# Kernel tuning notes

Hardware: AMD Instinct MI355X
Metric: run time of the kernel (lower is better)

Reference implementation:

```python
import jax, jax.numpy as jnp
import numpy as np

Q, B, D, NH, DH, DI, M = 1024, 4, 1024, 16, 64, 4096, 1024
K = Q + M  # klen
SCALE_W = 0.02
LN_EPS = 1e-5


def _layer_norm(x, g, b):
    mu = jnp.mean(x, axis=-1, keepdims=True)
    var = jnp.var(x, axis=-1, keepdims=True)
    return (x - mu) * jax.lax.rsqrt(var + LN_EPS) * g + b


def _rel_shift(x):
    # x: [qlen, klen, bsz, n_head] -> Transformer-XL relative shift
    q, k = x.shape[0], x.shape[1]
    zero_pad = jnp.zeros((q, 1) + x.shape[2:], x.dtype)
    x_padded = jnp.concatenate([zero_pad, x], axis=1)          # [q, k+1, b, n]
    x_padded = x_padded.reshape((k + 1, q) + x.shape[2:])      # [k+1, q, b, n]
    return x_padded[1:].reshape(x.shape)


def setup_inputs() -> dict:
    key = jax.random.key(0)
    ks = jax.random.split(key, 12)
    f32 = jnp.float32
    inp = {
        "w": jax.random.normal(ks[0], (Q, B, D), f32),
        "r": jax.random.normal(ks[1], (K, 1, D), f32),
        "mems": jax.random.normal(ks[2], (M, B, D), f32),
        "qkv_w": SCALE_W * jax.random.normal(ks[3], (D, 3 * NH * DH), f32),
        "r_net_w": SCALE_W * jax.random.normal(ks[4], (D, NH * DH), f32),
        "o_w": SCALE_W * jax.random.normal(ks[5], (NH * DH, D), f32),
        "r_w_bias": SCALE_W * jax.random.normal(ks[6], (NH, DH), f32),
        "r_r_bias": SCALE_W * jax.random.normal(ks[7], (NH, DH), f32),
        "ln1_g": jnp.ones((D,), f32),
        "ln1_b": jnp.zeros((D,), f32),
        "ff_w1": SCALE_W * jax.random.normal(ks[8], (D, DI), f32),
        "ff_b1": jnp.zeros((DI,), f32),
        "ff_w2": SCALE_W * jax.random.normal(ks[9], (DI, D), f32),
        "ff_b2": jnp.zeros((D,), f32),
        "ln2_g": jnp.ones((D,), f32),
        "ln2_b": jnp.zeros((D,), f32),
        # causal mask with memory: query i attends to keys j <= i + mem_len
        "attn_mask": jnp.arange(K)[None, :] > (jnp.arange(Q)[:, None] + M),
    }
    return inp


def reference(w, r, mems, qkv_w, r_net_w, o_w, r_w_bias, r_r_bias,
              ln1_g, ln1_b, ff_w1, ff_b1, ff_w2, ff_b2, ln2_g, ln2_b,
              attn_mask):
    qlen, bsz = w.shape[0], w.shape[1]
    # --- relative multi-head attention (post-lnorm, mems concat) ---
    cat = jnp.concatenate([mems, w], axis=0)                   # [klen, b, d]
    w_heads = cat @ qkv_w                                      # [klen, b, 3*nh*dh]
    r_head_k = (r @ r_net_w).reshape(-1, NH, DH)               # [rlen, nh, dh]
    q_h, k_h, v_h = jnp.split(w_heads, 3, axis=-1)
    klen = k_h.shape[0]
    q_h = q_h[-qlen:].reshape(qlen, bsz, NH, DH)
    k_h = k_h.reshape(klen, bsz, NH, DH)
    v_h = v_h.reshape(klen, bsz, NH, DH)

    rw_q = q_h + r_w_bias[None, None]                          # [q, b, nh, dh]
    AC = jnp.einsum('ibnd,jbnd->ijbn', rw_q, k_h)
    rr_q = q_h + r_r_bias[None, None]
    BD = jnp.einsum('ibnd,jnd->ijbn', rr_q, r_head_k)
    BD = _rel_shift(BD)

    scale = 1.0 / (DH ** 0.5)
    attn_score = (AC + BD) * scale                             # [q, k, b, nh]
    attn_score = jnp.where(attn_mask[:, :, None, None], -jnp.inf, attn_score)
    attn_prob = jax.nn.softmax(attn_score, axis=1)
    attn_vec = jnp.einsum('ijbn,jbnd->ibnd', attn_prob, v_h)
    attn_out = attn_vec.reshape(qlen, bsz, NH * DH) @ o_w      # [q, b, d]
    out = _layer_norm(w + attn_out, ln1_g, ln1_b)

    # --- position-wise FFN (post-lnorm) ---
    core = jax.nn.relu(out @ ff_w1 + ff_b1) @ ff_w2 + ff_b2
    out = _layer_norm(out + core, ln2_g, ln2_b)
    return out
```

## Files before the change

### kernel.cpp

```cpp
#include <hip/hip_runtime.h>
#include <math.h>


#define QLEN 1024
#define BSZ  4
#define DMODEL 1024
#define NHEAD 16
#define DHEAD 64
#define DINNER 4096
#define MEMLEN 1024
#define KLEN 2048

typedef __attribute__((ext_vector_type(8))) short short8;
typedef __attribute__((ext_vector_type(4))) short short4_t;
typedef __attribute__((ext_vector_type(4))) float f32x4;

__device__ __forceinline__ unsigned short f2bf(float x) {
  union { float f; unsigned u; } cv; cv.f = x;
  const unsigned u = cv.u;
  return (unsigned short)((u + 0x7FFFu + ((u >> 16) & 1u)) >> 16);
}
__device__ __forceinline__ float bf2f(unsigned short b) {
  union { unsigned u; float f; } cv; cv.u = ((unsigned)b) << 16;
  return cv.f;
}

__device__ __forceinline__ void gload16(const void* g, void* l) {
  __builtin_amdgcn_global_load_lds(
      (const __attribute__((address_space(1))) unsigned int*)g,
      (__attribute__((address_space(3))) unsigned int*)l, 16, 0, 0);
}

__device__ __forceinline__ int chidx(int row, int kc) {
  return row * 4 + (kc ^ ((row >> 1) & 3));
}

template<int MODE, int TN>
__global__ __launch_bounds__(256) void mgemm(
    const unsigned short* __restrict__ A, const unsigned short* __restrict__ Bt,
    float* __restrict__ C, unsigned short* __restrict__ Cb,
    const float* __restrict__ aux, const float* __restrict__ res,
    unsigned short* __restrict__ oK, unsigned short* __restrict__ oV,
    int Kdim, int N)
{
  constexpr int BUF = 8192 + TN * 64;
  __shared__ __align__(16) char smem[2 * BUF];

  const int tid = threadIdx.x;
  const int lane = tid & 63, wv = tid >> 6;

  const int gx = (int)gridDim.x;
  const int nwg = gx * (int)gridDim.y;
  const int flat = (int)blockIdx.y * gx + (int)blockIdx.x;
  const int swz = (flat & 7) * (nwg >> 3) + (flat >> 3);
  const int m0 = (swz / gx) * 128, n0 = (swz % gx) * TN;

  const unsigned short *gA0, *gA1, *gB0, *gB1 = nullptr;
  {
    int c = tid, m = c >> 2, kc = (c & 3) ^ ((m >> 1) & 3);
    gA0 = A + (size_t)(m0 + m) * Kdim + kc * 8;
    c = 256 + tid; m = c >> 2; kc = (c & 3) ^ ((m >> 1) & 3);
    gA1 = A + (size_t)(m0 + m) * Kdim + kc * 8;
    c = tid; int nn = c >> 2; kc = (c & 3) ^ ((nn >> 1) & 3);
    gB0 = Bt + (size_t)(n0 + nn) * Kdim + kc * 8;
    if constexpr (TN == 128) {
      c = 256 + tid; nn = c >> 2; kc = (c & 3) ^ ((nn >> 1) & 3);
      gB1 = Bt + (size_t)(n0 + nn) * Kdim + kc * 8;
    }
  }
  const int wvoff = (tid & 192) * 16;

  const int fr = lane & 15, kq = lane >> 4;
  constexpr int NJ = TN / 32;
  int aoff[4], boff[NJ];
#pragma unroll
  for (int t = 0; t < 4; ++t) {
    const int ra = (wv & 1) * 64 + t * 16 + fr;
    aoff[t] = chidx(ra, kq) * 16;
  }
#pragma unroll
  for (int t = 0; t < NJ; ++t) {
    const int rb = (wv >> 1) * (TN / 2) + t * 16 + fr;
    boff[t] = 8192 + chidx(rb, kq) * 16;
  }

  f32x4 acc[4][NJ] = {};

  {
    char* const b0 = smem + wvoff;
    gload16(gA0, b0);
    gload16(gA1, b0 + 4096);
    gload16(gB0, b0 + 8192);
    if constexpr (TN == 128) gload16(gB1, b0 + 12288);
    gA0 += 32; gA1 += 32; gB0 += 32;
    if constexpr (TN == 128) gB1 += 32;
  }

  int cur = 0;
  for (int k0 = 0; k0 < Kdim; k0 += 32) {
    if (k0 + 32 < Kdim) {
      char* const nb = smem + (cur ^ 1) * BUF + wvoff;
      gload16(gA0, nb);
      gload16(gA1, nb + 4096);
      gload16(gB0, nb + 8192);
      if constexpr (TN == 128) gload16(gB1, nb + 12288);
      gA0 += 32; gA1 += 32; gB0 += 32;
      if constexpr (TN == 128) gB1 += 32;
      if constexpr (TN == 128)
        asm volatile("s_waitcnt vmcnt(4)" ::: "memory");
      else
        asm volatile("s_waitcnt vmcnt(3)" ::: "memory");
    } else {
      asm volatile("s_waitcnt vmcnt(0)" ::: "memory");
    }
    __builtin_amdgcn_s_barrier();

    const char* const cb = smem + cur * BUF;
    short8 af[4], bfr[NJ];
#pragma unroll
    for (int t = 0; t < 4; ++t) af[t] = *(const short8*)(cb + aoff[t]);
#pragma unroll
    for (int t = 0; t < NJ; ++t) bfr[t] = *(const short8*)(cb + boff[t]);
#pragma unroll
    for (int i = 0; i < 4; ++i)
#pragma unroll
      for (int j = 0; j < NJ; ++j)
        acc[i][j] = __builtin_amdgcn_mfma_f32_16x16x32_bf16(
            af[i], bfr[j], acc[i][j], 0, 0, 0);

    asm volatile("s_waitcnt lgkmcnt(0)" ::: "memory");
    __builtin_amdgcn_s_barrier();
    cur ^= 1;
  }

  const int rbase = m0 + (wv & 1) * 64 + (lane >> 4) * 4;
  const int cbase = n0 + (wv >> 1) * (TN / 2) + (lane & 15);
#pragma unroll
  for (int i = 0; i < 4; ++i) {
#pragma unroll
    for (int r = 0; r < 4; ++r) {
      const int grow = rbase + i * 16 + r;
#pragma unroll
      for (int j = 0; j < NJ; ++j) {
        const int gcol = cbase + j * 16;
        const float v = acc[i][j][r];
        if constexpr (MODE == 0) {
          const int kkg = grow >> 2, b2 = grow & 3;
          const int sec = gcol >> 10, hn = (gcol >> 6) & 15, d = gcol & 63;
          const unsigned short bv = f2bf(v);
          if (sec == 0) {
            if (kkg >= MEMLEN)
              Cb[((size_t)(b2 * NHEAD + hn) * QLEN + (kkg - MEMLEN)) * DHEAD + d] = bv;
          } else if (sec == 1) {
            oK[((size_t)(b2 * NHEAD + hn) * KLEN + kkg) * DHEAD + d] = bv;
          } else {
            oV[((size_t)(b2 * NHEAD + hn) * KLEN + kkg) * DHEAD + d] = bv;
          }
        } else if constexpr (MODE == 1) {
          const int hn = gcol >> 6, d = gcol & 63;
          Cb[((size_t)hn * KLEN + grow) * DHEAD + d] = f2bf(v);
        } else if constexpr (MODE == 2) {
          C[(size_t)grow * N + gcol] = v + res[(size_t)grow * N + gcol];
        } else if constexpr (MODE == 3) {
          Cb[(size_t)grow * N + gcol] = f2bf(fmaxf(v + aux[gcol], 0.f));
        } else {
          C[(size_t)grow * N + gcol] = v + aux[gcol] + res[(size_t)grow * N + gcol];
        }
      }
    }
  }
}

__global__ __launch_bounds__(256) void transpose_v(
    const unsigned short* __restrict__ Vh, unsigned short* __restrict__ Vt)
{
  __shared__ unsigned short t[64 * 80];
  const int j0 = (int)blockIdx.x * 64;
  const int bn = (int)blockIdx.y;
  const int tid = threadIdx.x;
#pragma unroll
  for (int it = 0; it < 2; ++it) {
    const int f = it * 256 + tid;
    const int j = f >> 3, d8 = (f & 7) * 8;
    const short8 v = *(const short8*)(Vh + ((size_t)bn * KLEN + j0 + j) * DHEAD + d8);
    *(short8*)(t + j * 80 + d8) = v;
  }
  __syncthreads();
  const int d = tid >> 2, jseg = (tid & 3) * 16;
  short8 o0, o1;
#pragma unroll
  for (int e = 0; e < 8; ++e) o0[e] = (short)t[(jseg + e) * 80 + d];
#pragma unroll
  for (int e = 0; e < 8; ++e) o1[e] = (short)t[(jseg + 8 + e) * 80 + d];
  unsigned short* op = Vt + ((size_t)bn * DHEAD + d) * KLEN + j0 + jseg;
  *(short8*)op = o0;
  *(short8*)(op + 8) = o1;
}

__global__ __launch_bounds__(256) void cast_all(
    const float* __restrict__ mems, const float* __restrict__ w,
    const float* __restrict__ r, unsigned short* __restrict__ Xcat,
    unsigned short* __restrict__ Rb16)
{
  const size_t i = ((size_t)blockIdx.x * 256 + threadIdx.x) * 8;
  const float* src;
  unsigned short* dst;
  if (i < 4194304)       { src = mems + i;          dst = Xcat + i; }
  else if (i < 8388608)  { src = w + (i - 4194304); dst = Xcat + i; }
  else                   { src = r + (i - 8388608); dst = Rb16 + (i - 8388608); }
  const float4 x = *(const float4*)src;
  const float4 y = *(const float4*)(src + 4);
  short8 v;
  v[0] = (short)f2bf(x.x); v[1] = (short)f2bf(x.y);
  v[2] = (short)f2bf(x.z); v[3] = (short)f2bf(x.w);
  v[4] = (short)f2bf(y.x); v[5] = (short)f2bf(y.y);
  v[6] = (short)f2bf(y.z); v[7] = (short)f2bf(y.w);
  *(short8*)dst = v;
}

__global__ __launch_bounds__(256) void transpose_all(
    const float* __restrict__ qkv_w, const float* __restrict__ r_net_w,
    const float* __restrict__ o_w, const float* __restrict__ ff_w1,
    const float* __restrict__ ff_w2,
    unsigned short* __restrict__ Wqkv, unsigned short* __restrict__ Wr,
    unsigned short* __restrict__ Wo, unsigned short* __restrict__ W1,
    unsigned short* __restrict__ W2)
{
  const int bid = (int)blockIdx.x;
  const float* in; unsigned short* out; int R, C, xt, loc;
  if (bid < 768)        { in = qkv_w;   out = Wqkv; R = 1024; C = 3072; xt = 48; loc = bid; }
  else if (bid < 1024)  { in = r_net_w; out = Wr;   R = 1024; C = 1024; xt = 16; loc = bid - 768; }
  else if (bid < 1280)  { in = o_w;     out = Wo;   R = 1024; C = 1024; xt = 16; loc = bid - 1024; }
  else if (bid < 2304)  { in = ff_w1;   out = W1;   R = 1024; C = 4096; xt = 64; loc = bid - 1280; }
  else                  { in = ff_w2;   out = W2;   R = 4096; C = 1024; xt = 16; loc = bid - 2304; }
  const int c0 = (loc % xt) * 64, r0 = (loc / xt) * 64;

  __shared__ float t[64][65];
  const int tid = threadIdx.x;
  const int rr = tid >> 4, cc = (tid & 15) * 4;
#pragma unroll
  for (int it = 0; it < 4; ++it) {
    const int rw = rr + it * 16;
    const float4 v = *(const float4*)(in + (size_t)(r0 + rw) * C + c0 + cc);
    t[rw][cc] = v.x; t[rw][cc + 1] = v.y; t[rw][cc + 2] = v.z; t[rw][cc + 3] = v.w;
  }
  __syncthreads();
  const int oc = tid >> 2, ob = (tid & 3) * 16;
#pragma unroll
  for (int j4 = 0; j4 < 4; ++j4) {
    short4_t o;
#pragma unroll
    for (int j = 0; j < 4; ++j) o[j] = (short)f2bf(t[ob + j4 * 4 + j][oc]);
    *(short4_t*)(out + (size_t)(c0 + oc) * R + r0 + ob + j4 * 4) = o;
  }
}

__global__ __launch_bounds__(256, 2) void attn_mfma(
    const unsigned short* __restrict__ Qh, const unsigned short* __restrict__ Kh,
    const unsigned short* __restrict__ Vt, const unsigned short* __restrict__ Rk,
    const float* __restrict__ rwb, const float* __restrict__ rrb,
    float* __restrict__ Opart0, float* __restrict__ Opart1,
    float* __restrict__ den0, float* __restrict__ den1)
{
  __shared__ __align__(16) char smem[65536];

  const int tid = threadIdx.x;
  const int lane = tid & 63, wv = tid >> 6;
  const int quad = lane >> 4, l15 = lane & 15;

  const int bid0 = (int)blockIdx.y * 32 + (int)blockIdx.x;
  const int slot = bid0 >> 3;
  const int bn = (bid0 & 7) * 8 + (slot >> 5);
  const int inner = slot & 31;
  const int it = inner >> 1, sp = inner & 1;
  const int i0 = it * 64;
  const int n = bn & 15;

  const int nch = 17 + it;
  const int h = (nch + 1) >> 1;
  const int lo = sp ? h : 0, hi = sp ? nch : h;

  const unsigned short* __restrict__ Qb = Qh + (size_t)bn * QLEN * DHEAD;
  const unsigned short* __restrict__ Kb = Kh + (size_t)bn * KLEN * DHEAD;
  const unsigned short* __restrict__ Vb = Vt + (size_t)bn * DHEAD * KLEN;
  const unsigned short* __restrict__ Rb = Rk + (size_t)n * KLEN * DHEAD;

  short8 qk[2], qr[2];
  {
    const int qrow = i0 + wv * 16 + l15;
    const unsigned short* qp = Qb + (size_t)qrow * DHEAD + quad * 8;
    const float* wp = rwb + n * DHEAD + quad * 8;
    const float* rp = rrb + n * DHEAD + quad * 8;
#pragma unroll
    for (int ks = 0; ks < 2; ++ks) {
      const short8 q8 = *(const short8*)(qp + ks * 32);
#pragma unroll
      for (int e = 0; e < 8; ++e) {
        const float qv = bf2f((unsigned short)q8[e]);
        qk[ks][e] = (short)f2bf(qv + wp[ks * 32 + e]);
        qr[ks][e] = (short)f2bf(qv + rp[ks * 32 + e]);
      }
    }
  }

  int srcl[4];
  bool condE[4];
#pragma unroll
  for (int r = 0; r < 4; ++r) {
    const int E = l15 - quad * 4 - r + 15;
    srcl[r] = (lane & 48) | (E & 15);
    condE[r] = (E >= 16);
  }

  f32x4 O[4] = {};
  float rden[4] = {0.f, 0.f, 0.f, 0.f};
  const int wvoff = (tid & 192) * 16;

  {
    const int j0 = lo * 64;
    const int g64 = lo - it + 15;
    const int rb3 = (g64 % 3) * 64;
#pragma unroll
    for (int t2 = 0; t2 < 2; ++t2) {
      const int s = t2 * 256 + tid;
      const int row = s >> 3, kc = (s & 7) ^ (row & 7);
      gload16(Kb + (((size_t)(j0 + row)) << 6) + kc * 8,
              smem + t2 * 4096 + wvoff);
    }
#pragma unroll
    for (int t2 = 0; t2 < 2; ++t2) {
      const int s = t2 * 256 + tid;
      const int row = s >> 3, kc = (s & 7) ^ (row & 7);
      gload16(Vb + (((size_t)row) << 11) + j0 + kc * 8,
              smem + 16384 + t2 * 4096 + wvoff);
    }
    const int gw = j0 - i0 + 960;
#pragma unroll
    for (int t2 = 0; t2 < 4; ++t2) {
      const int rr = t2 * 32 + (tid >> 3);
      const int gr = gw + rr;
      const int kc = (tid & 7) ^ (rr & 7);
      int pb = rb3 + t2 * 32; if (pb >= 192) pb -= 192;
      gload16(Rb + (((size_t)gr) << 6) + kc * 8,
              smem + 32768 + pb * 128 + wvoff);
    }
  }

  int cur = 0;
  for (int ch = lo; ch < hi; ++ch) {
    const int j0 = ch * 64;
    const int g64 = ch - it + 15;
    const int rb3 = (g64 % 3) * 64;
    const int gw = j0 - i0 + 960;

    asm volatile("s_waitcnt lgkmcnt(0)" ::: "memory");
    __builtin_amdgcn_s_barrier();

    if (ch + 1 < hi) {
      const int nb = cur ^ 1;
      const int j0n = j0 + 64;
#pragma unroll
      for (int t2 = 0; t2 < 2; ++t2) {
        const int s = t2 * 256 + tid;
        const int row = s >> 3, kc = (s & 7) ^ (row & 7);
        gload16(Kb + (((size_t)(j0n + row)) << 6) + kc * 8,
                smem + nb * 8192 + t2 * 4096 + wvoff);
      }
#pragma unroll
      for (int t2 = 0; t2 < 2; ++t2) {
        const int s = t2 * 256 + tid;
        const int row = s >> 3, kc = (s & 7) ^ (row & 7);
        gload16(Vb + (((size_t)row) << 11) + j0n + kc * 8,
                smem + 16384 + nb * 8192 + t2 * 4096 + wvoff);
      }
#pragma unroll
      for (int t2 = 0; t2 < 2; ++t2) {
        const int rr = t2 * 32 + (tid >> 3);
        const int gr = gw + 128 + rr;
        const int kc = (tid & 7) ^ (rr & 7);
        int pb = rb3 + 128 + t2 * 32; if (pb >= 192) pb -= 192;
        gload16(Rb + (((size_t)gr) << 6) + kc * 8,
                smem + 32768 + pb * 128 + wvoff);
      }
      asm volatile("s_waitcnt vmcnt(6)" ::: "memory");
    } else {
      asm volatile("s_waitcnt vmcnt(0)" ::: "memory");
    }
    __builtin_amdgcn_s_barrier();

    const char* const kbase = smem + cur * 8192;
    const char* const vbase = smem + 16384 + cur * 8192;

    f32x4 sk[4];
#pragma unroll
    for (int jt = 0; jt < 4; ++jt) {
      f32x4 a = {0.f, 0.f, 0.f, 0.f};
#pragma unroll
      for (int ks = 0; ks < 2; ++ks) {
        const int frr = jt * 16 + l15;
        const int c = (ks * 4 + quad) ^ (l15 & 7);
        const short8 kf = *(const short8*)(kbase + (frr * 8 + c) * 16);
        a = __builtin_amdgcn_mfma_f32_16x16x32_bf16(qk[ks], kf, a, 0, 0, 0);
      }
      sk[jt] = a;
    }
    f32x4 uu[5];
#pragma unroll
    for (int s = 0; s < 5; ++s) {
      f32x4 a = {0.f, 0.f, 0.f, 0.f};
      int frr = rb3 + (3 - wv + s) * 16 + l15;
      if (frr >= 192) frr -= 192;
#pragma unroll
      for (int ks = 0; ks < 2; ++ks) {
        const int c = (ks * 4 + quad) ^ (l15 & 7);
        const short8 rf = *(const short8*)(smem + 32768 + (frr * 8 + c) * 16);
        a = __builtin_amdgcn_mfma_f32_16x16x32_bf16(qr[ks], rf, a, 0, 0, 0);
      }
      uu[s] = a;
    }

    float rot[5][4];
#pragma unroll
    for (int s = 0; s < 5; ++s)
#pragma unroll
      for (int r = 0; r < 4; ++r)
        rot[s][r] = __shfl(uu[s][r], srcl[r], 64);

    unsigned short* const Ps = (unsigned short*)(smem + 57344);
    constexpr float CE = 0.18033688f;
    const bool needmask = (ch - it) == 16;
#pragma unroll
    for (int jt = 0; jt < 4; ++jt) {
      const int jl = jt * 16 + l15;
#pragma unroll
      for (int r = 0; r < 4; ++r) {
        const int il = wv * 16 + quad * 4 + r;
        const float uv = condE[r] ? rot[jt + 1][r] : rot[jt][r];
        float p = exp2f((sk[jt][r] + uv) * CE);
        if (needmask) {
          const int dj = (j0 + jl) - (i0 + il);
          if (dj > 1024) p = 0.f;
        }
        rden[r] += p;
        Ps[(il * 8 + ((jl >> 3) ^ (il & 7))) * 8 + (jl & 7)] = f2bf(p);
      }
    }

#pragma unroll
    for (int ks = 0; ks < 2; ++ks) {
      const int frp = wv * 16 + l15;
      const int cp = (ks * 4 + quad) ^ (l15 & 7);
      const short8 pf = *(const short8*)(smem + 57344 + (frp * 8 + cp) * 16);
#pragma unroll
      for (int dt = 0; dt < 4; ++dt) {
        const int vr = dt * 16 + l15;
        const short8 vf = *(const short8*)(vbase + (vr * 8 + cp) * 16);
        O[dt] = __builtin_amdgcn_mfma_f32_16x16x32_bf16(pf, vf, O[dt], 0, 0, 0);
      }
    }
    cur ^= 1;
  }

#pragma unroll
  for (int m = 1; m < 16; m <<= 1)
#pragma unroll
    for (int r = 0; r < 4; ++r)
      rden[r] += __shfl_xor(rden[r], m, 64);

  float* const Op = sp ? Opart1 : Opart0;
  float* const dp = sp ? den1 : den0;
  const size_t ob = (size_t)(bn * 16 + it) * 64;
#pragma unroll
  for (int r = 0; r < 4; ++r) {
    const int il = wv * 16 + quad * 4 + r;
#pragma unroll
    for (int dt = 0; dt < 4; ++dt)
      Op[(ob + il) * 64 + dt * 16 + l15] = O[dt][r];
    if (l15 == 0) dp[ob + il] = rden[r];
  }
}

__global__ __launch_bounds__(256) void attn_combine(
    const float* __restrict__ O0, const float* __restrict__ O1,
    const float* __restrict__ d0, const float* __restrict__ d1,
    unsigned short* __restrict__ AVb)
{
  const int blk = (int)blockIdx.x;
  const int bn = blk >> 4, it = blk & 15;
  const int b = bn >> 4, n = bn & 15;
  const int tid = threadIdx.x;
  const int il = tid >> 2, ds = (tid & 3) * 16;
  const size_t base = ((size_t)blk * 64 + il) * 64 + ds;
  const float inv = 1.f / (d0[blk * 64 + il] + d1[blk * 64 + il]);
  short8 o0, o1;
#pragma unroll
  for (int g = 0; g < 2; ++g) {
    const float4 a = *(const float4*)(O0 + base + g * 8);
    const float4 bb = *(const float4*)(O1 + base + g * 8);
    const float4 a2 = *(const float4*)(O0 + base + g * 8 + 4);
    const float4 b2 = *(const float4*)(O1 + base + g * 8 + 4);
    short8& o = g ? o1 : o0;
    o[0] = (short)f2bf((a.x + bb.x) * inv);  o[1] = (short)f2bf((a.y + bb.y) * inv);
    o[2] = (short)f2bf((a.z + bb.z) * inv);  o[3] = (short)f2bf((a.w + bb.w) * inv);
    o[4] = (short)f2bf((a2.x + b2.x) * inv); o[5] = (short)f2bf((a2.y + b2.y) * inv);
    o[6] = (short)f2bf((a2.z + b2.z) * inv); o[7] = (short)f2bf((a2.w + b2.w) * inv);
  }
  unsigned short* op =
      AVb + ((size_t)(it * 64 + il) * BSZ + b) * DMODEL + n * DHEAD + ds;
  *(short8*)op = o0;
  *(short8*)(op + 8) = o1;
}

__global__ __launch_bounds__(256) void ln_kernel(
    float* __restrict__ X, const float* __restrict__ gw,
    const float* __restrict__ bw, unsigned short* __restrict__ bfo)
{
  const int row = blockIdx.x, tid = threadIdx.x;
  float* rp = X + (size_t)row * DMODEL;
  const float4 x = *(const float4*)(rp + tid * 4);
  float s = x.x + x.y + x.z + x.w;
  float q = x.x * x.x + x.y * x.y + x.z * x.z + x.w * x.w;
#pragma unroll
  for (int m = 1; m < 64; m <<= 1) {
    s += __shfl_xor(s, m, 64);
    q += __shfl_xor(q, m, 64);
  }
  __shared__ float ss[4], sq[4];
  if ((tid & 63) == 0) { ss[tid >> 6] = s; sq[tid >> 6] = q; }
  __syncthreads();
  s = ss[0] + ss[1] + ss[2] + ss[3];
  q = sq[0] + sq[1] + sq[2] + sq[3];
  const float mu = s * (1.f / DMODEL);
  const float var = q * (1.f / DMODEL) - mu * mu;
  const float rstd = rsqrtf(var + 1e-5f);
  const float4 g4 = *(const float4*)(gw + tid * 4);
  const float4 b4 = *(const float4*)(bw + tid * 4);
  float4 y;
  y.x = (x.x - mu) * rstd * g4.x + b4.x;
  y.y = (x.y - mu) * rstd * g4.y + b4.y;
  y.z = (x.z - mu) * rstd * g4.z + b4.z;
  y.w = (x.w - mu) * rstd * g4.w + b4.w;
  *(float4*)(rp + tid * 4) = y;
  if (bfo) {
    short4_t o;
    o[0] = (short)f2bf(y.x); o[1] = (short)f2bf(y.y);
    o[2] = (short)f2bf(y.z); o[3] = (short)f2bf(y.w);
    *(short4_t*)(bfo + (size_t)row * DMODEL + tid * 4) = o;
  }
}

extern "C" void kernel_launch(void* const* d_in, const int* in_sizes, int n_in,
                              void* d_out, int out_size, void* d_ws,
                              size_t ws_size, hipStream_t stream)
{
  const float* w       = (const float*)d_in[0];
  const float* r       = (const float*)d_in[1];
  const float* mems    = (const float*)d_in[2];
  const float* qkv_w   = (const float*)d_in[3];
  const float* r_net_w = (const float*)d_in[4];
  const float* o_w     = (const float*)d_in[5];
  const float* r_w_bias= (const float*)d_in[6];
  const float* r_r_bias= (const float*)d_in[7];
  const float* ln1_g   = (const float*)d_in[8];
  const float* ln1_b   = (const float*)d_in[9];
  const float* ff_w1   = (const float*)d_in[10];
  const float* ff_b1   = (const float*)d_in[11];
  const float* ff_w2   = (const float*)d_in[12];
  const float* ff_b2   = (const float*)d_in[13];
  const float* ln2_g   = (const float*)d_in[14];
  const float* ln2_b   = (const float*)d_in[15];
  float* out = (float*)d_out;

  float* X1 = (float*)d_ws;
  unsigned short* Qh   = (unsigned short*)(X1 + 4194304);
  unsigned short* Kh   = Qh + 4194304;
  unsigned short* Vt   = Kh + 8388608;
  unsigned short* Rk   = Vt + 8388608;
  unsigned short* Xcat = Rk + 2097152 + 8192;
  unsigned short* Wqkv = Xcat + 8388608;
  unsigned short* Wr   = Wqkv + 3145728;
  unsigned short* Wo   = Wr + 1048576;
  unsigned short* W1   = Wo + 1048576;
  unsigned short* W2   = W1 + 4194304;
  float* den0 = (float*)(W2 + 4194304);
  float* den1 = den0 + 65536;
  unsigned short* AVb  = (unsigned short*)(den1 + 65536);
  unsigned short* Vh     = (unsigned short*)X1;
  unsigned short* Rb16   = AVb;
  float* Opart0          = (float*)X1;
  float* Opart1          = (float*)Xcat;
  unsigned short* X1b    = Qh;
  unsigned short* H      = Kh;

  const dim3 blk(256);

  cast_all<<<dim3(5120), blk, 0, stream>>>(mems, w, r, Xcat, Rb16);
  transpose_all<<<dim3(3328), blk, 0, stream>>>(
      qkv_w, r_net_w, o_w, ff_w1, ff_w2, Wqkv, Wr, Wo, W1, W2);

  mgemm<0, 128><<<dim3(24, 64), blk, 0, stream>>>(
      Xcat, Wqkv, nullptr, Qh, nullptr, nullptr, Kh, Vh, DMODEL, 3 * DMODEL);
  transpose_v<<<dim3(32, 64), blk, 0, stream>>>(Vh, Vt);
  mgemm<1, 64><<<dim3(16, 16), blk, 0, stream>>>(
      Rb16, Wr, nullptr, Rk, nullptr, nullptr, nullptr, nullptr, DMODEL, DMODEL);
  attn_mfma<<<dim3(32, 64), blk, 0, stream>>>(
      Qh, Kh, Vt, Rk, r_w_bias, r_r_bias, Opart0, Opart1, den0, den1);
  attn_combine<<<dim3(1024), blk, 0, stream>>>(Opart0, Opart1, den0, den1, AVb);
  mgemm<2, 64><<<dim3(16, 32), blk, 0, stream>>>(
      AVb, Wo, X1, nullptr, nullptr, w, nullptr, nullptr, DMODEL, DMODEL);
  ln_kernel<<<dim3(4096), blk, 0, stream>>>(X1, ln1_g, ln1_b, X1b);
  mgemm<3, 128><<<dim3(32, 32), blk, 0, stream>>>(
      X1b, W1, nullptr, H, ff_b1, nullptr, nullptr, nullptr, DMODEL, DINNER);
  mgemm<4, 64><<<dim3(16, 32), blk, 0, stream>>>(
      H, W2, out, nullptr, ff_b2, X1, nullptr, nullptr, DINNER, DMODEL);
  ln_kernel<<<dim3(4096), blk, 0, stream>>>(out, ln2_g, ln2_b, nullptr);

  (void)in_sizes; (void)n_in; (void)out_size; (void)ws_size;
}
```

Measured before the change: 527.5 us.

## Add 256x256-tile 512-thread GEMM for QKV and FFN1 projections

Introduces a new GEMM kernel, mgemm2, that uses 512 threads, 256x256 output tiles, a 64KB double-buffered LDS, priority raising around MFMA bursts, and global loads issued after the fragment reads. It replaces the 128x128 GEMM for the QKV projection and the first FFN layer, which are the two widest GEMMs, to raise data reuse per loaded byte. The attention softmax exponent is rewritten from exp2f with a folded constant to __expf of a scaled score. The larger tiles cut the grid to 384 and 256 workgroups and increase register pressure, which may reduce occupancy and wave-count balance.

```diff
diff --git a/kernel.cpp b/kernel.cpp
--- a/kernel.cpp
+++ b/kernel.cpp
@@ -35,114 +35,101 @@
   return row * 4 + (kc ^ ((row >> 1) & 3));
 }
 
-template<int MODE, int TN>
-__global__ __launch_bounds__(256) void mgemm(
+template<int MODE>
+__global__ __launch_bounds__(512, 2) void mgemm2(
     const unsigned short* __restrict__ A, const unsigned short* __restrict__ Bt,
-    float* __restrict__ C, unsigned short* __restrict__ Cb,
-    const float* __restrict__ aux, const float* __restrict__ res,
+    unsigned short* __restrict__ Cb, const float* __restrict__ aux,
     unsigned short* __restrict__ oK, unsigned short* __restrict__ oV,
     int Kdim, int N)
 {
-  constexpr int BUF = 8192 + TN * 64;
-  __shared__ __align__(16) char smem[2 * BUF];
+  __shared__ __align__(16) char smem[65536];
 
   const int tid = threadIdx.x;
   const int lane = tid & 63, wv = tid >> 6;
+  const int wr = wv >> 2, wc = wv & 3;
+  const int quad = lane >> 4, l15 = lane & 15;
 
   const int gx = (int)gridDim.x;
   const int nwg = gx * (int)gridDim.y;
   const int flat = (int)blockIdx.y * gx + (int)blockIdx.x;
   const int swz = (flat & 7) * (nwg >> 3) + (flat >> 3);
-  const int m0 = (swz / gx) * 128, n0 = (swz % gx) * TN;
-
-  const unsigned short *gA0, *gA1, *gB0, *gB1 = nullptr;
-  {
-    int c = tid, m = c >> 2, kc = (c & 3) ^ ((m >> 1) & 3);
-    gA0 = A + (size_t)(m0 + m) * Kdim + kc * 8;
-    c = 256 + tid; m = c >> 2; kc = (c & 3) ^ ((m >> 1) & 3);
-    gA1 = A + (size_t)(m0 + m) * Kdim + kc * 8;
-    c = tid; int nn = c >> 2; kc = (c & 3) ^ ((nn >> 1) & 3);
-    gB0 = Bt + (size_t)(n0 + nn) * Kdim + kc * 8;
-    if constexpr (TN == 128) {
-      c = 256 + tid; nn = c >> 2; kc = (c & 3) ^ ((nn >> 1) & 3);
-      gB1 = Bt + (size_t)(n0 + nn) * Kdim + kc * 8;
-    }
-  }
-  const int wvoff = (tid & 192) * 16;
-
-  const int fr = lane & 15, kq = lane >> 4;
-  constexpr int NJ = TN / 32;
-  int aoff[4], boff[NJ];
-#pragma unroll
-  for (int t = 0; t < 4; ++t) {
-    const int ra = (wv & 1) * 64 + t * 16 + fr;
-    aoff[t] = chidx(ra, kq) * 16;
-  }
-#pragma unroll
-  for (int t = 0; t < NJ; ++t) {
-    const int rb = (wv >> 1) * (TN / 2) + t * 16 + fr;
-    boff[t] = 8192 + chidx(rb, kq) * 16;
-  }
-
-  f32x4 acc[4][NJ] = {};
-
-  {
-    char* const b0 = smem + wvoff;
-    gload16(gA0, b0);
-    gload16(gA1, b0 + 4096);
-    gload16(gB0, b0 + 8192);
-    if constexpr (TN == 128) gload16(gB1, b0 + 12288);
-    gA0 += 32; gA1 += 32; gB0 += 32;
-    if constexpr (TN == 128) gB1 += 32;
-  }
-
-  int cur = 0;
-  for (int k0 = 0; k0 < Kdim; k0 += 32) {
-    if (k0 + 32 < Kdim) {
-      char* const nb = smem + (cur ^ 1) * BUF + wvoff;
-      gload16(gA0, nb);
-      gload16(gA1, nb + 4096);
-      gload16(gB0, nb + 8192);
-      if constexpr (TN == 128) gload16(gB1, nb + 12288);
-      gA0 += 32; gA1 += 32; gB0 += 32;
-      if constexpr (TN == 128) gB1 += 32;
-      if constexpr (TN == 128)
-        asm volatile("s_waitcnt vmcnt(4)" ::: "memory");
-      else
-        asm volatile("s_waitcnt vmcnt(3)" ::: "memory");
-    } else {
-      asm volatile("s_waitcnt vmcnt(0)" ::: "memory");
-    }
+  const int m0 = (swz / gx) * 256, n0 = (swz % gx) * 256;
+
+  const int srow = tid >> 2;
+  const int skc = (tid & 3) ^ (srow & 3);
+  const unsigned short* pA0 = A + (size_t)(m0 + srow) * Kdim + skc * 8;
+  const unsigned short* pA1 = A + (size_t)(m0 + 128 + srow) * Kdim + skc * 8;
+  const unsigned short* pB0 = Bt + (size_t)(n0 + srow) * Kdim + skc * 8;
+  const unsigned short* pB1 = Bt + (size_t)(n0 + 128 + srow) * Kdim + skc * 8;
+  const int wb = (tid & 448) * 16;
+
+  const int cch = (quad ^ (l15 & 3)) * 16;
+  const int aoffb = wr * 8192 + l15 * 64 + cch;
+  const int boffb = 32768 + (wc >> 1) * 8192 +
+                    ((wc & 1) * 64 + l15) * 64 + cch;
+
+  f32x4 acc[8][4] = {};
+
+  const int nkt = Kdim >> 5;
+  gload16(pA0, smem + wb);
+  gload16(pA1, smem + 8192 + wb);
+  gload16(pB0, smem + 32768 + wb);
+  gload16(pB1, smem + 40960 + wb);
+  pA0 += 32; pA1 += 32; pB0 += 32; pB1 += 32;
+
+  for (int kt = 0; kt < nkt; ++kt) {
+    const int bo = (kt & 1) * 16384;
+    asm volatile("s_waitcnt vmcnt(0)" ::: "memory");
     __builtin_amdgcn_s_barrier();
 
-    const char* const cb = smem + cur * BUF;
-    short8 af[4], bfr[NJ];
-#pragma unroll
-    for (int t = 0; t < 4; ++t) af[t] = *(const short8*)(cb + aoff[t]);
-#pragma unroll
-    for (int t = 0; t < NJ; ++t) bfr[t] = *(const short8*)(cb + boff[t]);
+    short8 bfr[4], af[4];
+#pragma unroll
+    for (int j = 0; j < 4; ++j)
+      bfr[j] = *(const short8*)(smem + bo + boffb + j * 1024);
 #pragma unroll
     for (int i = 0; i < 4; ++i)
-#pragma unroll
-      for (int j = 0; j < NJ; ++j)
+      af[i] = *(const short8*)(smem + bo + aoffb + i * 1024);
+    if (kt + 1 < nkt) {
+      const int nb = bo ^ 16384;
+      gload16(pA0, smem + nb + wb);
+      gload16(pA1, smem + nb + 8192 + wb);
+      gload16(pB0, smem + 32768 + nb + wb);
+      gload16(pB1, smem + 40960 + nb + wb);
+      pA0 += 32; pA1 += 32; pB0 += 32; pB1 += 32;
+    }
+    __builtin_amdgcn_s_setprio(1);
+#pragma unroll
+    for (int i = 0; i < 4; ++i)
+#pragma unroll
+      for (int j = 0; j < 4; ++j)
         acc[i][j] = __builtin_amdgcn_mfma_f32_16x16x32_bf16(
             af[i], bfr[j], acc[i][j], 0, 0, 0);
-
-    asm volatile("s_waitcnt lgkmcnt(0)" ::: "memory");
+    __builtin_amdgcn_s_setprio(0);
     __builtin_amdgcn_s_barrier();
-    cur ^= 1;
-  }
-
-  const int rbase = m0 + (wv & 1) * 64 + (lane >> 4) * 4;
-  const int cbase = n0 + (wv >> 1) * (TN / 2) + (lane & 15);
-#pragma unroll
-  for (int i = 0; i < 4; ++i) {
+
+#pragma unroll
+    for (int i = 0; i < 4; ++i)
+      af[i] = *(const short8*)(smem + bo + aoffb + (i + 4) * 1024);
+    __builtin_amdgcn_s_setprio(1);
+#pragma unroll
+    for (int i = 0; i < 4; ++i)
+#pragma unroll
+      for (int j = 0; j < 4; ++j)
+        acc[i + 4][j] = __builtin_amdgcn_mfma_f32_16x16x32_bf16(
+            af[i], bfr[j], acc[i + 4][j], 0, 0, 0);
+    __builtin_amdgcn_s_setprio(0);
+  }
+
+  const int rb0 = m0 + wr * 128 + quad * 4;
+  const int cb0 = n0 + wc * 64 + l15;
+#pragma unroll
+  for (int i = 0; i < 8; ++i) {
 #pragma unroll
     for (int r = 0; r < 4; ++r) {
-      const int grow = rbase + i * 16 + r;
-#pragma unroll
-      for (int j = 0; j < NJ; ++j) {
-        const int gcol = cbase + j * 16;
+      const int grow = rb0 + i * 16 + r;
+#pragma unroll
+      for (int j = 0; j < 4; ++j) {
+        const int gcol = cb0 + j * 16;
         const float v = acc[i][j][r];
         if constexpr (MODE == 0) {
           const int kkg = grow >> 2, b2 = grow & 3;
@@ -156,13 +143,116 @@
           } else {
             oV[((size_t)(b2 * NHEAD + hn) * KLEN + kkg) * DHEAD + d] = bv;
           }
-        } else if constexpr (MODE == 1) {
+        } else {
+          Cb[(size_t)grow * N + gcol] = f2bf(fmaxf(v + aux[gcol], 0.f));
+        }
+      }
+    }
+  }
+}
+
+template<int MODE, int TN>
+__global__ __launch_bounds__(256) void mgemm(
+    const unsigned short* __restrict__ A, const unsigned short* __restrict__ Bt,
+    float* __restrict__ C, unsigned short* __restrict__ Cb,
+    const float* __restrict__ aux, const float* __restrict__ res,
+    int Kdim, int N)
+{
+  constexpr int BUF = 8192 + TN * 64;
+  __shared__ __align__(16) char smem[2 * BUF];
+
+  const int tid = threadIdx.x;
+  const int lane = tid & 63, wv = tid >> 6;
+
+  const int gx = (int)gridDim.x;
+  const int nwg = gx * (int)gridDim.y;
+  const int flat = (int)blockIdx.y * gx + (int)blockIdx.x;
+  const int swz = (flat & 7) * (nwg >> 3) + (flat >> 3);
+  const int m0 = (swz / gx) * 128, n0 = (swz % gx) * TN;
+
+  const unsigned short *gA0, *gA1, *gB0;
+  {
+    int c = tid, m = c >> 2, kc = (c & 3) ^ ((m >> 1) & 3);
+    gA0 = A + (size_t)(m0 + m) * Kdim + kc * 8;
+    c = 256 + tid; m = c >> 2; kc = (c & 3) ^ ((m >> 1) & 3);
+    gA1 = A + (size_t)(m0 + m) * Kdim + kc * 8;
+    c = tid; int nn = c >> 2; kc = (c & 3) ^ ((nn >> 1) & 3);
+    gB0 = Bt + (size_t)(n0 + nn) * Kdim + kc * 8;
+  }
+  const int wvoff = (tid & 192) * 16;
+
+  const int fr = lane & 15, kq = lane >> 4;
+  constexpr int NJ = TN / 32;
+  int aoff[4], boff[NJ];
+#pragma unroll
+  for (int t = 0; t < 4; ++t) {
+    const int ra = (wv & 1) * 64 + t * 16 + fr;
+    aoff[t] = chidx(ra, kq) * 16;
+  }
+#pragma unroll
+  for (int t = 0; t < NJ; ++t) {
+    const int rb = (wv >> 1) * (TN / 2) + t * 16 + fr;
+    boff[t] = 8192 + chidx(rb, kq) * 16;
+  }
+
+  f32x4 acc[4][NJ] = {};
+
+  {
+    char* const b0 = smem + wvoff;
+    gload16(gA0, b0);
+    gload16(gA1, b0 + 4096);
+    gload16(gB0, b0 + 8192);
+    gA0 += 32; gA1 += 32; gB0 += 32;
+  }
+
+  int cur = 0;
+  for (int k0 = 0; k0 < Kdim; k0 += 32) {
+    if (k0 + 32 < Kdim) {
+      char* const nb = smem + (cur ^ 1) * BUF + wvoff;
+      gload16(gA0, nb);
+      gload16(gA1, nb + 4096);
+      gload16(gB0, nb + 8192);
+      gA0 += 32; gA1 += 32; gB0 += 32;
+      asm volatile("s_waitcnt vmcnt(3)" ::: "memory");
+    } else {
+      asm volatile("s_waitcnt vmcnt(0)" ::: "memory");
+    }
+    __builtin_amdgcn_s_barrier();
+
+    const char* const cb = smem + cur * BUF;
+    short8 af[4], bfr[NJ];
+#pragma unroll
+    for (int t = 0; t < 4; ++t) af[t] = *(const short8*)(cb + aoff[t]);
+#pragma unroll
+    for (int t = 0; t < NJ; ++t) bfr[t] = *(const short8*)(cb + boff[t]);
+#pragma unroll
+    for (int i = 0; i < 4; ++i)
+#pragma unroll
+      for (int j = 0; j < NJ; ++j)
+        acc[i][j] = __builtin_amdgcn_mfma_f32_16x16x32_bf16(
+            af[i], bfr[j], acc[i][j], 0, 0, 0);
+
+    asm volatile("s_waitcnt lgkmcnt(0)" ::: "memory");
+    __builtin_amdgcn_s_barrier();
+    cur ^= 1;
+  }
+
+  const int rbase = m0 + (wv & 1) * 64 + (lane >> 4) * 4;
+  const int cbase = n0 + (wv >> 1) * (TN / 2) + (lane & 15);
+#pragma unroll
+  for (int i = 0; i < 4; ++i) {
+#pragma unroll
+    for (int r = 0; r < 4; ++r) {
+      const int grow = rbase + i * 16 + r;
+#pragma unroll
+      for (int j = 0; j < NJ; ++j) {
+        const int gcol = cbase + j * 16;
+        const float v = acc[i][j][r];
+        if constexpr (MODE == 1) {
           const int hn = gcol >> 6, d = gcol & 63;
           Cb[((size_t)hn * KLEN + grow) * DHEAD + d] = f2bf(v);
         } else if constexpr (MODE == 2) {
           C[(size_t)grow * N + gcol] = v + res[(size_t)grow * N + gcol];
-        } else if constexpr (MODE == 3) {
-          Cb[(size_t)grow * N + gcol] = f2bf(fmaxf(v + aux[gcol], 0.f));
         } else {
           C[(size_t)grow * N + gcol] = v + aux[gcol] + res[(size_t)grow * N + gcol];
         }
@@ -427,7 +517,6 @@
         rot[s][r] = __shfl(uu[s][r], srcl[r], 64);
 
     unsigned short* const Ps = (unsigned short*)(smem + 57344);
-    constexpr float CE = 0.18033688f;
     const bool needmask = (ch - it) == 16;
 #pragma unroll
     for (int jt = 0; jt < 4; ++jt) {
@@ -436,7 +525,8 @@
       for (int r = 0; r < 4; ++r) {
         const int il = wv * 16 + quad * 4 + r;
         const float uv = condE[r] ? rot[jt + 1][r] : rot[jt][r];
-        float p = exp2f((sk[jt][r] + uv) * CE);
+        const float sv = (sk[jt][r] + uv) * 0.125f;
+        float p = __expf(sv);
         if (needmask) {
           const int dj = (j0 + jl) - (i0 + il);
           if (dj > 1024) p = 0.f;
@@ -593,26 +683,27 @@
   unsigned short* H      = Kh;
 
   const dim3 blk(256);
+  const dim3 blk2(512);
 
   cast_all<<<dim3(5120), blk, 0, stream>>>(mems, w, r, Xcat, Rb16);
   transpose_all<<<dim3(3328), blk, 0, stream>>>(
       qkv_w, r_net_w, o_w, ff_w1, ff_w2, Wqkv, Wr, Wo, W1, W2);
 
-  mgemm<0, 128><<<dim3(24, 64), blk, 0, stream>>>(
-      Xcat, Wqkv, nullptr, Qh, nullptr, nullptr, Kh, Vh, DMODEL, 3 * DMODEL);
+  mgemm2<0><<<dim3(12, 32), blk2, 0, stream>>>(
+      Xcat, Wqkv, Qh, nullptr, Kh, Vh, DMODEL, 3 * DMODEL);
   transpose_v<<<dim3(32, 64), blk, 0, stream>>>(Vh, Vt);
   mgemm<1, 64><<<dim3(16, 16), blk, 0, stream>>>(
-      Rb16, Wr, nullptr, Rk, nullptr, nullptr, nullptr, nullptr, DMODEL, DMODEL);
+      Rb16, Wr, nullptr, Rk, nullptr, nullptr, DMODEL, DMODEL);
   attn_mfma<<<dim3(32, 64), blk, 0, stream>>>(
       Qh, Kh, Vt, Rk, r_w_bias, r_r_bias, Opart0, Opart1, den0, den1);
   attn_combine<<<dim3(1024), blk, 0, stream>>>(Opart0, Opart1, den0, den1, AVb);
   mgemm<2, 64><<<dim3(16, 32), blk, 0, stream>>>(
-      AVb, Wo, X1, nullptr, nullptr, w, nullptr, nullptr, DMODEL, DMODEL);
+      AVb, Wo, X1, nullptr, nullptr, w, DMODEL, DMODEL);
   ln_kernel<<<dim3(4096), blk, 0, stream>>>(X1, ln1_g, ln1_b, X1b);
-  mgemm<3, 128><<<dim3(32, 32), blk, 0, stream>>>(
-      X1b, W1, nullptr, H, ff_b1, nullptr, nullptr, nullptr, DMODEL, DINNER);
+  mgemm2<3><<<dim3(16, 16), blk2, 0, stream>>>(
+      X1b, W1, H, ff_b1, nullptr, nullptr, DMODEL, DINNER);
   mgemm<4, 64><<<dim3(16, 32), blk, 0, stream>>>(
-      H, W2, out, nullptr, ff_b2, X1, nullptr, nullptr, DINNER, DMODEL);
+      H, W2, out, nullptr, ff_b2, X1, DINNER, DMODEL);
   ln_kernel<<<dim3(4096), blk, 0, stream>>>(out, ln2_g, ln2_b, nullptr);
 
   (void)in_sizes; (void)n_in; (void)out_size; (void)ws_size;
```

After: 527.9 us. No clear change (+0.1%).
